# Kernel optimization log

Hardware: AMD Instinct MI355X
Metric: run time of the kernel (lower is better)

Reference implementation:

```python
import jax, jax.numpy as jnp
import numpy as np

N_NODES = 20000
IN_FEAT = 128
CONV_OUT = 32
N_EDGES = 640000
FC1_OUT = 128


def setup_inputs() -> dict:
    key = jax.random.key(0)
    ks = jax.random.split(key, 8)
    x = jax.random.normal(ks[0], (N_NODES, IN_FEAT), dtype=jnp.float32)
    edge_index = jax.random.randint(ks[1], (2, N_EDGES), 0, N_NODES, dtype=jnp.int64)
    # GCNConv params (PyG: lin weight [in, out] applied as x @ W, plus bias)
    w_conv = jax.random.normal(ks[2], (IN_FEAT, CONV_OUT), dtype=jnp.float32) * (1.0 / np.sqrt(IN_FEAT))
    b_conv = jnp.zeros((CONV_OUT,), dtype=jnp.float32)
    # fc1: Linear(32*N -> 128), torch stores weight as [out, in]
    w_fc1 = jax.random.normal(ks[3], (FC1_OUT, CONV_OUT * N_NODES), dtype=jnp.float32) * (1.0 / np.sqrt(CONV_OUT * N_NODES))
    b_fc1 = jnp.zeros((FC1_OUT,), dtype=jnp.float32)
    # fc2: Linear(128 -> N)
    w_fc2 = jax.random.normal(ks[4], (N_NODES, FC1_OUT), dtype=jnp.float32) * (1.0 / np.sqrt(FC1_OUT))
    b_fc2 = jnp.zeros((N_NODES,), dtype=jnp.float32)
    return {"x": x, "edge_index": edge_index, "w_conv": w_conv, "b_conv": b_conv,
            "w_fc1": w_fc1, "b_fc1": b_fc1, "w_fc2": w_fc2, "b_fc2": b_fc2}


def gcn_conv(x, edge_index, w, b):
    # PyG GCNConv default: add self-loops, symmetric normalization D^-1/2 (A+I) D^-1/2
    n = x.shape[0]
    loop = jnp.arange(n, dtype=edge_index.dtype)
    src = jnp.concatenate([edge_index[0], loop])  # [E+N]
    dst = jnp.concatenate([edge_index[1], loop])
    deg = jax.ops.segment_sum(jnp.ones_like(dst, dtype=x.dtype), dst, num_segments=n)
    dinv = jnp.where(deg > 0, jax.lax.rsqrt(deg), 0.0)
    norm = dinv[src] * dinv[dst]  # [E+N]
    h = x @ w  # [N, out] — transform before propagate
    msg = h[src] * norm[:, None]  # gather
    agg = jax.ops.segment_sum(msg, dst, num_segments=n)  # scatter-add
    return agg + b


def reference(x, edge_index, w_conv, b_conv, w_fc1, b_fc1, w_fc2, b_fc2):
    h1 = jax.nn.relu(gcn_conv(x, edge_index, w_conv, b_conv))  # [N, 32]; dropout inactive (eval)
    flat = h1.reshape(-1, CONV_OUT * N_NODES)  # [1, 32*N]
    h3 = jax.nn.relu(flat @ w_fc1.T + b_fc1)   # [1, 128]
    out = jax.nn.relu(h3 @ w_fc2.T + b_fc2)    # [1, N] q-values
    return out
```

## Files before the change

kernel.cpp:

```cpp
#include <hip/hip_runtime.h>

#define N_NODES 20000
#define IN_FEAT 128
#define CONV_OUT 32
#define N_EDGES 640000
#define FC1_OUT 128


#define ZERO_WORDS 20000

__global__ __launch_bounds__(256) void k_zero(float4* __restrict__ p) {
    int i = blockIdx.x * 256 + threadIdx.x;
    if (i < ZERO_WORDS / 4) p[i] = make_float4(0.f, 0.f, 0.f, 0.f);
}

__global__ __launch_bounds__(256) void k_degslot(const int* __restrict__ ei,
                                                 int* __restrict__ cnt,
                                                 int* __restrict__ r) {
    int e = blockIdx.x * 256 + threadIdx.x;
    if (e < N_EDGES) {
        int d = ei[N_EDGES + e];
        r[e] = atomicAdd(&cnt[d], 1);
    }
}

#define SCAN_T 1024
#define SCAN_CHUNK 20
__global__ __launch_bounds__(1024) void k_scan(const int* __restrict__ cnt,
                                               int* __restrict__ startv,
                                               float* __restrict__ dinv) {
    __shared__ int ld[SCAN_T * SCAN_CHUNK];
    __shared__ int ps[SCAN_T];
    int t = threadIdx.x;
    const int4* c4 = (const int4*)cnt;
    int4* l4 = (int4*)ld;
    #pragma unroll
    for (int i = 0; i < 5; ++i) {
        int idx = i * SCAN_T + t;
        l4[idx] = (idx < N_NODES / 4) ? c4[idx] : make_int4(0, 0, 0, 0);
    }
    __syncthreads();
    int local[SCAN_CHUNK];
    int base = t * SCAN_CHUNK;
    int sum = 0;
    #pragma unroll
    for (int i = 0; i < SCAN_CHUNK; ++i) { local[i] = ld[base + i]; sum += local[i]; }
    ps[t] = sum;
    __syncthreads();
    for (int off = 1; off < SCAN_T; off <<= 1) {
        int v = (t >= off) ? ps[t - off] : 0;
        __syncthreads();
        ps[t] += v;
        __syncthreads();
    }
    int run = (t == 0) ? 0 : ps[t - 1];
    #pragma unroll
    for (int i = 0; i < SCAN_CHUNK; ++i) {
        int n = base + i;
        ld[n] = run;
        if (n < N_NODES) dinv[n] = rsqrtf((float)local[i] + 1.0f);
        run += local[i];
    }
    __syncthreads();
    int4* s4 = (int4*)startv;
    #pragma unroll
    for (int i = 0; i < 5; ++i) {
        int idx = i * SCAN_T + t;
        if (idx < N_NODES / 4) s4[idx] = l4[idx];
    }
    if (t == 0) startv[N_NODES] = N_EDGES;
}

__global__ __launch_bounds__(256) void k_gemm1(const float* __restrict__ x,
                                               const float* __restrict__ w,
                                               const float* __restrict__ dinv,
                                               float* __restrict__ h) {
    __shared__ float xs[64][132];
    __shared__ float ws[128][32];
    int tid = threadIdx.x;
    int n0 = blockIdx.x * 64;

    const float4* w4 = (const float4*)w;
    float4* ws4 = (float4*)ws;
    #pragma unroll
    for (int i = 0; i < 4; ++i) ws4[i * 256 + tid] = w4[i * 256 + tid];

    const float4* x4 = (const float4*)x;
    #pragma unroll
    for (int i = 0; i < 8; ++i) {
        int idx = i * 256 + tid;
        int nl  = idx >> 5;
        int k4  = idx & 31;
        int n   = n0 + nl;
        float4 v = make_float4(0.f, 0.f, 0.f, 0.f);
        if (n < N_NODES) v = x4[(size_t)n * 32 + k4];
        *(float4*)&xs[nl][k4 * 4] = v;
    }
    __syncthreads();

    int c4  = tid & 7;
    int nl0 = tid >> 3;
    const float4* wsrow = (const float4*)ws;
    #pragma unroll
    for (int p = 0; p < 2; ++p) {
        int nl = nl0 + p * 32;
        float4 acc = make_float4(0.f, 0.f, 0.f, 0.f);
        #pragma unroll 8
        for (int k = 0; k < 128; k += 4) {
            float4 xv  = *(const float4*)&xs[nl][k];
            float4 wv0 = wsrow[(k + 0) * 8 + c4];
            float4 wv1 = wsrow[(k + 1) * 8 + c4];
            float4 wv2 = wsrow[(k + 2) * 8 + c4];
            float4 wv3 = wsrow[(k + 3) * 8 + c4];
            acc.x += xv.x * wv0.x + xv.y * wv1.x + xv.z * wv2.x + xv.w * wv3.x;
            acc.y += xv.x * wv0.y + xv.y * wv1.y + xv.z * wv2.y + xv.w * wv3.y;
            acc.z += xv.x * wv0.z + xv.y * wv1.z + xv.z * wv2.z + xv.w * wv3.z;
            acc.w += xv.x * wv0.w + xv.y * wv1.w + xv.z * wv2.w + xv.w * wv3.w;
        }
        int n = n0 + nl;
        if (n < N_NODES) {
            float dv = dinv[n];
            acc.x *= dv; acc.y *= dv; acc.z *= dv; acc.w *= dv;
            *(float4*)&h[(size_t)n * 32 + c4 * 4] = acc;
        }
    }
}

__global__ __launch_bounds__(256) void k_fill(const int* __restrict__ ei,
                                              const int* __restrict__ startv,
                                              const int* __restrict__ r,
                                              int* __restrict__ csr) {
    int e = blockIdx.x * 256 + threadIdx.x;
    if (e < N_EDGES) {
        int s = ei[e];
        int d = ei[N_EDGES + e];
        csr[startv[d] + r[e]] = s;
    }
}

__global__ __launch_bounds__(256) void k_gather(const int* __restrict__ startv,
                                                const int* __restrict__ csr,
                                                const float* __restrict__ h,
                                                const float* __restrict__ dinv,
                                                const float* __restrict__ bc,
                                                float* __restrict__ flat) {
    int tid  = threadIdx.x;
    int lane = tid & 63;
    int n    = blockIdx.x * 4 + (tid >> 6);
    if (n >= N_NODES) return;
    int es = lane >> 3;
    int f4 = lane & 7;
    const float4* h4 = (const float4*)h;
    float4 acc = make_float4(0.f, 0.f, 0.f, 0.f);
    int p0 = startv[n], p1 = startv[n + 1];
    #pragma unroll 2
    for (int p = p0 + es; p < p1; p += 8) {
        int s = csr[p];
        float4 v = h4[(size_t)s * 8 + f4];
        acc.x += v.x; acc.y += v.y; acc.z += v.z; acc.w += v.w;
    }
    #pragma unroll
    for (int m = 8; m < 64; m <<= 1) {
        acc.x += __shfl_xor(acc.x, m);
        acc.y += __shfl_xor(acc.y, m);
        acc.z += __shfl_xor(acc.z, m);
        acc.w += __shfl_xor(acc.w, m);
    }
    if (lane < 8) {
        float4 self = h4[(size_t)n * 8 + f4];
        float dv = dinv[n];
        float4 b = ((const float4*)bc)[f4];
        float4 r_;
        r_.x = fmaxf((acc.x + self.x) * dv + b.x, 0.f);
        r_.y = fmaxf((acc.y + self.y) * dv + b.y, 0.f);
        r_.z = fmaxf((acc.z + self.z) * dv + b.z, 0.f);
        r_.w = fmaxf((acc.w + self.w) * dv + b.w, 0.f);
        ((float4*)flat)[(size_t)n * 8 + f4] = r_;
    }
}

#define FC1_CH 25
__global__ __launch_bounds__(256) void k_fc1(const float* __restrict__ flat,
                                             const float* __restrict__ w,
                                             float* __restrict__ part) {
    int bid = blockIdx.x;
    int jg = bid & 31;
    int ch = bid >> 5;
    int j0 = jg * 4;
    const float4* f4 = (const float4*)flat;
    const float4* w0 = (const float4*)(w + (size_t)(j0 + 0) * (CONV_OUT * N_NODES));
    const float4* w1 = (const float4*)(w + (size_t)(j0 + 1) * (CONV_OUT * N_NODES));
    const float4* w2 = (const float4*)(w + (size_t)(j0 + 2) * (CONV_OUT * N_NODES));
    const float4* w3 = (const float4*)(w + (size_t)(j0 + 3) * (CONV_OUT * N_NODES));
    int base = ch * 6400;
    float a0 = 0.f, a1 = 0.f, a2 = 0.f, a3 = 0.f;
    #pragma unroll 5
    for (int it = 0; it < 25; ++it) {
        int k = base + it * 256 + threadIdx.x;
        float4 fv  = f4[k];
        float4 v0  = w0[k];
        float4 v1  = w1[k];
        float4 v2  = w2[k];
        float4 v3  = w3[k];
        a0 += v0.x * fv.x + v0.y * fv.y + v0.z * fv.z + v0.w * fv.w;
        a1 += v1.x * fv.x + v1.y * fv.y + v1.z * fv.z + v1.w * fv.w;
        a2 += v2.x * fv.x + v2.y * fv.y + v2.z * fv.z + v2.w * fv.w;
        a3 += v3.x * fv.x + v3.y * fv.y + v3.z * fv.z + v3.w * fv.w;
    }
    #pragma unroll
    for (int o = 32; o > 0; o >>= 1) {
        a0 += __shfl_down(a0, o);
        a1 += __shfl_down(a1, o);
        a2 += __shfl_down(a2, o);
        a3 += __shfl_down(a3, o);
    }
    __shared__ float red[4][4];
    int wv = threadIdx.x >> 6;
    if ((threadIdx.x & 63) == 0) {
        red[wv][0] = a0; red[wv][1] = a1; red[wv][2] = a2; red[wv][3] = a3;
    }
    __syncthreads();
    if (threadIdx.x < 4) {
        float s = red[0][threadIdx.x] + red[1][threadIdx.x] +
                  red[2][threadIdx.x] + red[3][threadIdx.x];
        part[(size_t)(j0 + threadIdx.x) * FC1_CH + ch] = s;
    }
}

__global__ __launch_bounds__(256) void k_fc2(const float* __restrict__ part,
                                             const float* __restrict__ b1,
                                             const float* __restrict__ w2,
                                             const float* __restrict__ b2,
                                             float* __restrict__ out) {
    __shared__ float h3s[128];
    int tid = threadIdx.x;
    if (tid < 128) {
        const float* p = part + (size_t)tid * FC1_CH;
        float s = 0.f;
        #pragma unroll
        for (int i = 0; i < FC1_CH; ++i) s += p[i];
        h3s[tid] = fmaxf(s + b1[tid], 0.f);
    }
    __syncthreads();
    int i = blockIdx.x * 256 + tid;
    if (i < N_NODES) {
        const float4* wr = (const float4*)(w2 + (size_t)i * FC1_OUT);
        const float4* h4 = (const float4*)h3s;
        float acc = b2[i];
        #pragma unroll
        for (int j = 0; j < 32; ++j) {
            float4 wv = wr[j];
            float4 hv = h4[j];
            acc += wv.x * hv.x + wv.y * hv.y + wv.z * hv.z + wv.w * hv.w;
        }
        out[i] = fmaxf(acc, 0.f);
    }
}

extern "C" void kernel_launch(void* const* d_in, const int* in_sizes, int n_in,
                              void* d_out, int out_size, void* d_ws, size_t ws_size,
                              hipStream_t stream) {
    const float* x      = (const float*)d_in[0];
    const int*   ei     = (const int*)d_in[1];
    const float* w_conv = (const float*)d_in[2];
    const float* b_conv = (const float*)d_in[3];
    const float* w_fc1  = (const float*)d_in[4];
    const float* b_fc1  = (const float*)d_in[5];
    const float* w_fc2  = (const float*)d_in[6];
    const float* b_fc2  = (const float*)d_in[7];
    float* ws = (float*)d_ws;
    int*   cnt    = (int*)ws;
    float* part   = ws + 20000;
    int*   startv = (int*)(ws + 23200);
    float* dinv   = ws + 43204;
    int*   r      = (int*)(ws + 63204);
    int*   csr    = (int*)(ws + 703204);
    float* h      = ws + 1343204;
    float* flat   = ws + 1983204;
    float* out    = (float*)d_out;

    k_zero<<<(ZERO_WORDS / 4 + 255) / 256, 256, 0, stream>>>((float4*)d_ws);
    k_degslot<<<(N_EDGES + 255) / 256, 256, 0, stream>>>(ei, cnt, r);
    k_scan<<<1, SCAN_T, 0, stream>>>(cnt, startv, dinv);
    k_gemm1<<<(N_NODES + 63) / 64, 256, 0, stream>>>(x, w_conv, dinv, h);
    k_fill<<<(N_EDGES + 255) / 256, 256, 0, stream>>>(ei, startv, r, csr);
    k_gather<<<(N_NODES + 3) / 4, 256, 0, stream>>>(startv, csr, h, dinv, b_conv, flat);
    k_fc1<<<32 * FC1_CH, 256, 0, stream>>>(flat, w_fc1, part);
    k_fc2<<<(N_NODES + 255) / 256, 256, 0, stream>>>(part, b_fc1, w_fc2, b_fc2, out);
}
```

Before: 165.7 us.

## Replicate degree counters across sixteen slots to reduce atomic contention

The per-node degree counters used while building the CSR are split into sixteen replicas, chosen by the low bits of the edge index, so concurrent atomicAdds on the same destination are spread over separate addresses. The single-block scan now sums the replicas for each node and writes per-replica prefix offsets, which the fill kernel adds when placing each edge. The cost is a sixteen-times larger zeroing pass, a single workgroup reading all replicas through uncoalesced strided loads, and an extra offset array read in the fill kernel.

```diff
diff --git a/kernel.cpp b/kernel.cpp
--- a/kernel.cpp
+++ b/kernel.cpp
@@ -5,9 +5,10 @@
 #define CONV_OUT 32
 #define N_EDGES 640000
 #define FC1_OUT 128
-
-
-#define ZERO_WORDS 20000
+#define NREP 16
+
+
+#define ZERO_WORDS 320000
 
 __global__ __launch_bounds__(256) void k_zero(float4* __restrict__ p) {
     int i = blockIdx.x * 256 + threadIdx.x;
@@ -20,7 +21,7 @@
     int e = blockIdx.x * 256 + threadIdx.x;
     if (e < N_EDGES) {
         int d = ei[N_EDGES + e];
-        r[e] = atomicAdd(&cnt[d], 1);
+        r[e] = atomicAdd(&cnt[(e & (NREP - 1)) * N_NODES + d], 1);
     }
 }
 
@@ -28,23 +29,36 @@
 #define SCAN_CHUNK 20
 __global__ __launch_bounds__(1024) void k_scan(const int* __restrict__ cnt,
                                                int* __restrict__ startv,
+                                               int* __restrict__ roff,
                                                float* __restrict__ dinv) {
     __shared__ int ld[SCAN_T * SCAN_CHUNK];
     __shared__ int ps[SCAN_T];
     int t = threadIdx.x;
-    const int4* c4 = (const int4*)cnt;
-    int4* l4 = (int4*)ld;
-    #pragma unroll
-    for (int i = 0; i < 5; ++i) {
-        int idx = i * SCAN_T + t;
-        l4[idx] = (idx < N_NODES / 4) ? c4[idx] : make_int4(0, 0, 0, 0);
-    }
-    __syncthreads();
+    int base = t * SCAN_CHUNK;
     int local[SCAN_CHUNK];
-    int base = t * SCAN_CHUNK;
     int sum = 0;
-    #pragma unroll
-    for (int i = 0; i < SCAN_CHUNK; ++i) { local[i] = ld[base + i]; sum += local[i]; }
+    #pragma unroll 1
+    for (int i = 0; i < SCAN_CHUNK; ++i) {
+        int n = base + i;
+        int deg = 0;
+        if (n < N_NODES) {
+            int acc = 0;
+            int off[NREP];
+            #pragma unroll
+            for (int k = 0; k < NREP; ++k) {
+                int c = cnt[k * N_NODES + n];
+                off[k] = acc;
+                acc += c;
+            }
+            deg = acc;
+            int4* ro = (int4*)&roff[n * NREP];
+            #pragma unroll
+            for (int k = 0; k < NREP / 4; ++k)
+                ro[k] = make_int4(off[k*4], off[k*4+1], off[k*4+2], off[k*4+3]);
+        }
+        local[i] = deg;
+        sum += deg;
+    }
     ps[t] = sum;
     __syncthreads();
     for (int off = 1; off < SCAN_T; off <<= 1) {
@@ -62,6 +76,7 @@
         run += local[i];
     }
     __syncthreads();
+    const int4* l4 = (const int4*)ld;
     int4* s4 = (int4*)startv;
     #pragma unroll
     for (int i = 0; i < 5; ++i) {
@@ -128,13 +143,14 @@
 
 __global__ __launch_bounds__(256) void k_fill(const int* __restrict__ ei,
                                               const int* __restrict__ startv,
+                                              const int* __restrict__ roff,
                                               const int* __restrict__ r,
                                               int* __restrict__ csr) {
     int e = blockIdx.x * 256 + threadIdx.x;
     if (e < N_EDGES) {
         int s = ei[e];
         int d = ei[N_EDGES + e];
-        csr[startv[d] + r[e]] = s;
+        csr[startv[d] + roff[d * NREP + (e & (NREP - 1))] + r[e]] = s;
     }
 }
 
@@ -188,10 +204,11 @@
     int ch = bid >> 5;
     int j0 = jg * 4;
     const float4* f4 = (const float4*)flat;
-    const float4* w0 = (const float4*)(w + (size_t)(j0 + 0) * (CONV_OUT * N_NODES));
-    const float4* w1 = (const float4*)(w + (size_t)(j0 + 1) * (CONV_OUT * N_NODES));
-    const float4* w2 = (const float4*)(w + (size_t)(j0 + 2) * (CONV_OUT * N_NODES));
-    const float4* w3 = (const float4*)(w + (size_t)(j0 + 3) * (CONV_OUT * N_NODES));
+    const size_t row4 = (size_t)CONV_OUT * N_NODES / 4;
+    const float4* w0 = (const float4*)w + (size_t)(j0 + 0) * row4;
+    const float4* w1 = (const float4*)w + (size_t)(j0 + 1) * row4;
+    const float4* w2 = (const float4*)w + (size_t)(j0 + 2) * row4;
+    const float4* w3 = (const float4*)w + (size_t)(j0 + 3) * row4;
     int base = ch * 6400;
     float a0 = 0.f, a1 = 0.f, a2 = 0.f, a3 = 0.f;
     #pragma unroll 5
@@ -270,20 +287,21 @@
     const float* b_fc2  = (const float*)d_in[7];
     float* ws = (float*)d_ws;
     int*   cnt    = (int*)ws;
-    float* part   = ws + 20000;
-    int*   startv = (int*)(ws + 23200);
-    float* dinv   = ws + 43204;
-    int*   r      = (int*)(ws + 63204);
-    int*   csr    = (int*)(ws + 703204);
-    float* h      = ws + 1343204;
-    float* flat   = ws + 1983204;
+    float* part   = ws + 320000;
+    int*   startv = (int*)(ws + 323200);
+    float* dinv   = ws + 343204;
+    int*   roff   = (int*)(ws + 363204);
+    int*   r      = (int*)(ws + 683204);
+    int*   csr    = (int*)(ws + 1323204);
+    float* h      = ws + 1963204;
+    float* flat   = ws + 2603204;
     float* out    = (float*)d_out;
 
     k_zero<<<(ZERO_WORDS / 4 + 255) / 256, 256, 0, stream>>>((float4*)d_ws);
     k_degslot<<<(N_EDGES + 255) / 256, 256, 0, stream>>>(ei, cnt, r);
-    k_scan<<<1, SCAN_T, 0, stream>>>(cnt, startv, dinv);
+    k_scan<<<1, SCAN_T, 0, stream>>>(cnt, startv, roff, dinv);
     k_gemm1<<<(N_NODES + 63) / 64, 256, 0, stream>>>(x, w_conv, dinv, h);
-    k_fill<<<(N_EDGES + 255) / 256, 256, 0, stream>>>(ei, startv, r, csr);
+    k_fill<<<(N_EDGES + 255) / 256, 256, 0, stream>>>(ei, startv, roff, r, csr);
     k_gather<<<(N_NODES + 3) / 4, 256, 0, stream>>>(startv, csr, h, dinv, b_conv, flat);
     k_fc1<<<32 * FC1_CH, 256, 0, stream>>>(flat, w_fc1, part);
     k_fc2<<<(N_NODES + 255) / 256, 256, 0, stream>>>(part, b_fc1, w_fc2, b_fc2, out);
```

Measured after the change: 322.4 us. 1.95x slower.
